# Performance work log

Measured on AMD Instinct MI355X. Metric: run time of the kernel, lower is better.

The kernel has to match this reference:

```python
import jax, jax.numpy as jnp
import numpy as np

NOISE_EPS = 1e-2


def setup_inputs() -> dict:
    key = jax.random.key(0)
    ks = jax.random.split(key, 6)
    N, D, E, H = 16384, 512, 8, 1024
    x = jax.random.normal(ks[0], (N, D), jnp.float32)
    eps = jax.random.normal(ks[1], (N, E), jnp.float32)
    w_gate = jax.random.normal(ks[2], (D, E), jnp.float32) * 0.02
    w_noise = jax.random.normal(ks[3], (D, E), jnp.float32) * 0.02
    W_h = jnp.eye(E, dtype=jnp.float32)  # module initializes W_h = eye(num_experts)
    W1 = jax.random.normal(ks[4], (E, D, H), jnp.float32) * 0.02
    b1 = jnp.zeros((E, H), jnp.float32)
    W2 = jax.random.normal(ks[5], (E, H, D), jnp.float32) * 0.02
    b2 = jnp.zeros((E, D), jnp.float32)
    return dict(x=x, eps=eps, w_gate=w_gate, w_noise=w_noise, W_h=W_h,
                W1=W1, b1=b1, W2=W2, b2=b2, k=2, capacity=5120)


def reference(x, eps, w_gate, w_noise, W_h, W1, b1, W2, b2, k, capacity):
    N, D = x.shape
    E = w_gate.shape[1]
    # --- noisy top-k gating ---
    clean_logits = (x @ w_gate) @ W_h                       # [N, E]
    noise_stddev = jax.nn.softplus(x @ w_noise) + NOISE_EPS  # [N, E]
    noisy_logits = clean_logits + eps * noise_stddev
    top_vals, top_idx = jax.lax.top_k(noisy_logits, k)       # [N, k]
    top_gates = jax.nn.softmax(top_vals, axis=-1)
    gates = jnp.zeros((N, E), x.dtype).at[jnp.arange(N)[:, None], top_idx].set(top_gates)
    # --- capacity masking: keep the first `capacity` routed tokens per expert (batch order) ---
    active = gates > 0
    rank = jnp.cumsum(active, axis=0) - 1                    # per-expert arrival rank
    keep = active & (rank < capacity)
    gates = jnp.where(keep, gates, jnp.zeros((), x.dtype))
    # --- dispatch into fixed [E, capacity] buffers (dummy slot absorbs dropped writes) ---
    flat = jnp.where(keep, jnp.arange(E)[None, :] * capacity + rank, E * capacity)  # [N, E]
    tok = jnp.broadcast_to(jnp.arange(N, dtype=jnp.int32)[:, None], (N, E))
    buf = jnp.zeros(E * capacity + 1, jnp.int32).at[flat].set(tok)[:E * capacity].reshape(E, capacity)
    gbuf = jnp.zeros(E * capacity + 1, x.dtype).at[flat].set(gates)[:E * capacity].reshape(E, capacity)
    x_exp = x[buf]                                           # [E, C, D] gather
    # --- per-expert 1-layer FFN (grouped GEMM) ---
    h = jax.nn.relu(jnp.einsum('ecd,edh->ech', x_exp, W1) + b1[:, None, :])
    y_exp = jnp.einsum('ech,eho->eco', h, W2) + b2[:, None, :]
    # --- weighted scatter-combine (unfilled slots have gate 0, so they add nothing) ---
    weighted = y_exp * gbuf[..., None]
    combined = jnp.zeros((N, D), x.dtype).at[buf.reshape(-1)].add(weighted.reshape(-1, D))
    return combined
```

## Files before the change

kernel.cpp:

```cpp
#include <hip/hip_runtime.h>
#include <hip/hip_bf16.h>
#include <cstdint>

#define NTOK 16384
#define DIM 512
#define NEXP 8
#define HID 1024
#define CAPACITY 5120

typedef __attribute__((ext_vector_type(8))) short bf16x8;
typedef __attribute__((ext_vector_type(4))) float f32x4;
typedef unsigned long long u64;

__device__ __forceinline__ unsigned short f2bf(float f) {
    unsigned u = __float_as_uint(f);
    unsigned r = (u + 0x7FFFu + ((u >> 16) & 1u)) >> 16;
    return (unsigned short)r;
}

#define GLDS16(gp, lp) __builtin_amdgcn_global_load_lds( \
    (const __attribute__((address_space(1))) void*)(gp), \
    (__attribute__((address_space(3))) void*)(lp), 16, 0, 0)

__global__ __launch_bounds__(256) void gating_kernel(
    const float* __restrict__ x, const float* __restrict__ eps,
    const float* __restrict__ wg, const float* __restrict__ wn,
    const float* __restrict__ Wh, int2* __restrict__ rec)
{
    int w = threadIdx.x >> 6, lane = threadIdx.x & 63;
    int n = blockIdx.x * 4 + w;
    float ag[8], an[8];
#pragma unroll
    for (int e = 0; e < 8; ++e) { ag[e] = 0.f; an[e] = 0.f; }
    const float* xr = x + (size_t)n * DIM;
#pragma unroll
    for (int i = 0; i < DIM / 64; ++i) {
        int d = i * 64 + lane;
        float xv = xr[d];
        const float4* g4 = reinterpret_cast<const float4*>(wg + (size_t)d * 8);
        const float4* n4 = reinterpret_cast<const float4*>(wn + (size_t)d * 8);
        float4 a0 = g4[0], a1 = g4[1], b0 = n4[0], b1v = n4[1];
        ag[0] += xv * a0.x; ag[1] += xv * a0.y; ag[2] += xv * a0.z; ag[3] += xv * a0.w;
        ag[4] += xv * a1.x; ag[5] += xv * a1.y; ag[6] += xv * a1.z; ag[7] += xv * a1.w;
        an[0] += xv * b0.x; an[1] += xv * b0.y; an[2] += xv * b0.z; an[3] += xv * b0.w;
        an[4] += xv * b1v.x; an[5] += xv * b1v.y; an[6] += xv * b1v.z; an[7] += xv * b1v.w;
    }
#pragma unroll
    for (int off = 32; off; off >>= 1) {
#pragma unroll
        for (int e = 0; e < 8; ++e) {
            ag[e] += __shfl_xor(ag[e], off);
            an[e] += __shfl_xor(an[e], off);
        }
    }
    float noisy[8];
#pragma unroll
    for (int e = 0; e < 8; ++e) {
        float c = 0.f;
#pragma unroll
        for (int j = 0; j < 8; ++j) c += ag[j] * Wh[j * 8 + e];
        float v = an[e];
        float sp = fmaxf(v, 0.f) + log1pf(expf(-fabsf(v)));
        noisy[e] = c + eps[(size_t)n * 8 + e] * (sp + 1e-2f);
    }
    int i1 = 0; float v1 = noisy[0];
#pragma unroll
    for (int e = 1; e < 8; ++e) if (noisy[e] > v1) { v1 = noisy[e]; i1 = e; }
    int i2 = -1; float v2 = -3.4e38f;
#pragma unroll
    for (int e = 0; e < 8; ++e) if (e != i1 && noisy[e] > v2) { v2 = noisy[e]; i2 = e; }
    float ex = expf(v2 - v1);
    float g1 = 1.f / (1.f + ex);
    if (lane == 0)
        rec[n] = make_int2(i1 | (i2 << 8), __float_as_int(g1));
}

__global__ __launch_bounds__(1024) void scan_local(
    const int2* __restrict__ rec, unsigned* __restrict__ lrank, int* __restrict__ btot)
{
    __shared__ u64 wtot[16];
    __shared__ int wprefix[16][8];
    int tid = threadIdx.x, w = tid >> 6, lane = tid & 63;
    int n = blockIdx.x * 1024 + tid;
    int2 r = rec[n];
    int e1 = r.x & 0xFF, e2 = (r.x >> 8) & 0xFF;
    u64 m = (1ULL << (e1 * 8)) | (1ULL << (e2 * 8));
    u64 incl = m;
#pragma unroll
    for (int off = 1; off < 64; off <<= 1) {
        u64 v = __shfl_up(incl, off);
        if (lane >= off) incl += v;
    }
    if (lane == 63) wtot[w] = incl;
    __syncthreads();
    if (tid < 128) {
        int e = tid & 7, ww = tid >> 3;
        int s = 0;
        for (int j = 0; j < ww; ++j) s += (int)((wtot[j] >> (e * 8)) & 0xFF);
        wprefix[ww][e] = s;
        if (ww == 15)
            btot[blockIdx.x * 8 + e] = s + (int)((wtot[15] >> (e * 8)) & 0xFF);
    }
    __syncthreads();
    u64 excl = incl - m;
    unsigned l1 = (unsigned)(wprefix[w][e1] + (int)((excl >> (e1 * 8)) & 0xFF));
    unsigned l2 = (unsigned)(wprefix[w][e2] + (int)((excl >> (e2 * 8)) & 0xFF));
    lrank[n] = l1 | (l2 << 16);
}

__global__ __launch_bounds__(64) void scan_offs(
    const int* __restrict__ btot, int* __restrict__ off, int* __restrict__ counts,
    const int* __restrict__ cap_p)
{
    int e = threadIdx.x;
    if (e >= 8) return;
    int cap = *cap_p; if (cap > CAPACITY) cap = CAPACITY;
    int run = 0;
    for (int b = 0; b < 16; ++b) {
        off[b * 8 + e] = run;
        run += btot[b * 8 + e];
    }
    counts[e] = min(run, cap);
}

__global__ __launch_bounds__(1024) void scatter_k(
    const int2* __restrict__ rec, const unsigned* __restrict__ lrank,
    const int* __restrict__ off, const int* __restrict__ cap_p,
    int* __restrict__ buf, float* __restrict__ gbuf)
{
    int tid = threadIdx.x, b = blockIdx.x;
    int n = b * 1024 + tid;
    int cap = *cap_p; if (cap > CAPACITY) cap = CAPACITY;
    int2 r = rec[n];
    int e1 = r.x & 0xFF, e2 = (r.x >> 8) & 0xFF;
    float g1 = __int_as_float(r.y), g2 = 1.f - g1;
    unsigned lr = lrank[n];
    int r1 = off[b * 8 + e1] + (int)(lr & 0xFFFF);
    int r2 = off[b * 8 + e2] + (int)(lr >> 16);
    if (r1 < cap) { buf[e1 * CAPACITY + r1] = n; gbuf[e1 * CAPACITY + r1] = g1; }
    if (r2 < cap) { buf[e2 * CAPACITY + r2] = n; gbuf[e2 * CAPACITY + r2] = g2; }
}

__global__ __launch_bounds__(256) void gather_x(
    const float* __restrict__ x, const int* __restrict__ buf,
    const int* __restrict__ counts, unsigned short* __restrict__ xe)
{
    int slot = blockIdx.x * 4 + (threadIdx.x >> 6);
    int d0 = (threadIdx.x & 63) * 8;
    int e = slot / CAPACITY, rr = slot - e * CAPACITY;
    int4 v = make_int4(0, 0, 0, 0);
    if (rr < counts[e]) {
        int tok = buf[slot];
        const float* src = x + (size_t)tok * DIM + d0;
        float4 a = *reinterpret_cast<const float4*>(src);
        float4 b = *reinterpret_cast<const float4*>(src + 4);
        v.x = f2bf(a.x) | ((int)f2bf(a.y) << 16);
        v.y = f2bf(a.z) | ((int)f2bf(a.w) << 16);
        v.z = f2bf(b.x) | ((int)f2bf(b.y) << 16);
        v.w = f2bf(b.z) | ((int)f2bf(b.w) << 16);
    }
    *reinterpret_cast<int4*>(xe + (size_t)slot * DIM + d0) = v;
}

__global__ __launch_bounds__(256) void tcvt(const float* __restrict__ in,
                                            unsigned short* __restrict__ out, int R, int C)
{
    __shared__ float tile[32][33];
    int z = blockIdx.z;
    int c0 = blockIdx.x * 32, r0 = blockIdx.y * 32;
    int tx = threadIdx.x, ty = threadIdx.y;
    const float* inz = in + (size_t)z * R * C;
    unsigned short* outz = out + (size_t)z * R * C;
#pragma unroll
    for (int j = 0; j < 32; j += 8)
        tile[ty + j][tx] = inz[(size_t)(r0 + ty + j) * C + c0 + tx];
    __syncthreads();
#pragma unroll
    for (int j = 0; j < 32; j += 8)
        outz[(size_t)(c0 + ty + j) * R + r0 + tx] = f2bf(tile[tx][ty + j]);
}

template <int MODE>
__global__ __launch_bounds__(256, 4) void ffn_gemm(
    const unsigned short* __restrict__ A, const unsigned short* __restrict__ Bt,
    const float* __restrict__ bias, unsigned short* __restrict__ Hout,
    float* __restrict__ Out, const int* __restrict__ buf,
    const float* __restrict__ gbuf, const int* __restrict__ counts,
    int Ka, int Nd)
{
    int flat = blockIdx.x + gridDim.x * (blockIdx.y + gridDim.y * blockIdx.z);
    int e  = flat & 7;
    int rr = flat >> 3;
    int tn = rr % gridDim.y;
    int tm = rr / gridDim.y;

    int cnt = counts[e];
    if (tm * 128 >= cnt) return;
    int tid = threadIdx.x, w = tid >> 6, lane = tid & 63;
    int q = lane >> 4, rl = lane & 15;

    __shared__ __align__(16) char lds[32768];
    char* As = lds;
    char* Bs = lds + 16384;

    unsigned aoff[4], boff[4];
#pragma unroll
    for (int i = 0; i < 4; ++i) {
        int p = (w * 4 + i) * 64 + lane;
        int row = p >> 3, kp = p & 7;
        int c = kp ^ (row & 7);
        aoff[i] = (unsigned)(e * CAPACITY + tm * 128 + row) * Ka + c * 8;
        boff[i] = (unsigned)(e * Nd + tn * 128 + row) * Ka + c * 8;
    }

    f32x4 acc[4][4];
#pragma unroll
    for (int mi = 0; mi < 4; ++mi)
#pragma unroll
        for (int ni = 0; ni < 4; ++ni)
            acc[mi][ni] = (f32x4){0.f, 0.f, 0.f, 0.f};

    int wm = w >> 1, wn = w & 1;

    for (int k0 = 0; k0 < Ka; k0 += 64) {
#pragma unroll
        for (int i = 0; i < 4; ++i) {
            GLDS16(A + aoff[i] + k0, As + (w * 4 + i) * 1024);
            GLDS16(Bt + boff[i] + k0, Bs + (w * 4 + i) * 1024);
        }
        __syncthreads();
#pragma unroll
        for (int kk = 0; kk < 2; ++kk) {
            bf16x8 af[4], bfr[4];
#pragma unroll
            for (int mi = 0; mi < 4; ++mi) {
                int row = wm * 64 + mi * 16 + rl;
                int cc = (kk * 4 + q) ^ (row & 7);
                af[mi] = *reinterpret_cast<const bf16x8*>(As + row * 128 + cc * 16);
            }
#pragma unroll
            for (int ni = 0; ni < 4; ++ni) {
                int row = wn * 64 + ni * 16 + rl;
                int cc = (kk * 4 + q) ^ (row & 7);
                bfr[ni] = *reinterpret_cast<const bf16x8*>(Bs + row * 128 + cc * 16);
            }
#pragma unroll
            for (int mi = 0; mi < 4; ++mi)
#pragma unroll
                for (int ni = 0; ni < 4; ++ni)
                    acc[mi][ni] = __builtin_amdgcn_mfma_f32_16x16x32_bf16(
                        af[mi], bfr[ni], acc[mi][ni], 0, 0, 0);
        }
        __syncthreads();
    }

    if (MODE == 1) {
#pragma unroll
        for (int ni = 0; ni < 4; ++ni) {
            int gcol = tn * 128 + wn * 64 + ni * 16 + rl;
            float bv = bias[e * Nd + gcol];
#pragma unroll
            for (int mi = 0; mi < 4; ++mi) {
#pragma unroll
                for (int r = 0; r < 4; ++r) {
                    int grow = tm * 128 + wm * 64 + mi * 16 + q * 4 + r;
                    float v = fmaxf(acc[mi][ni][r] + bv, 0.f);
                    Hout[(size_t)(e * CAPACITY + grow) * HID + gcol] = f2bf(v);
                }
            }
        }
    } else {
        int ebase = e * CAPACITY;
#pragma unroll
        for (int ni = 0; ni < 4; ++ni) {
            int gcol = tn * 128 + wn * 64 + ni * 16 + rl;
            float bv = bias[e * Nd + gcol];
#pragma unroll
            for (int mi = 0; mi < 4; ++mi) {
#pragma unroll
                for (int r = 0; r < 4; ++r) {
                    int grow = tm * 128 + wm * 64 + mi * 16 + q * 4 + r;
                    if (grow < cnt) {
                        int tok = buf[ebase + grow];
                        float g = gbuf[ebase + grow];
                        float v = (acc[mi][ni][r] + bv) * g;
                        atomicAdd(Out + (size_t)tok * DIM + gcol, v);
                    }
                }
            }
        }
    }
}

extern "C" void kernel_launch(void* const* d_in, const int* in_sizes, int n_in,
                              void* d_out, int out_size, void* d_ws, size_t ws_size,
                              hipStream_t stream)
{
    const float* x   = (const float*)d_in[0];
    const float* eps = (const float*)d_in[1];
    const float* wg  = (const float*)d_in[2];
    const float* wn  = (const float*)d_in[3];
    const float* Wh  = (const float*)d_in[4];
    const float* W1  = (const float*)d_in[5];
    const float* b1  = (const float*)d_in[6];
    const float* W2  = (const float*)d_in[7];
    const float* b2  = (const float*)d_in[8];
    const int* capp  = (const int*)d_in[10];

    char* ws = (char*)d_ws;
    unsigned short* xe   = (unsigned short*)(ws);
    unsigned short* w1t  = (unsigned short*)(ws + 41943040);
    unsigned short* w2t  = (unsigned short*)(ws + 50331648);
    unsigned short* hK   = (unsigned short*)(ws + 58720256);
    int*      buf    = (int*)     (ws + 142606336);
    float*    gbuf   = (float*)   (ws + 142770176);
    int2*     rec    = (int2*)    (ws + 142934016);
    unsigned* lrank  = (unsigned*)(ws + 143065088);
    int*      btot   = (int*)     (ws + 143130624);
    int*      off    = (int*)     (ws + 143131136);
    int*      counts = (int*)     (ws + 143131648);

    float* out = (float*)d_out;
    hipMemsetAsync(out, 0, (size_t)out_size * sizeof(float), stream);

    gating_kernel<<<NTOK / 4, 256, 0, stream>>>(x, eps, wg, wn, Wh, rec);
    scan_local<<<16, 1024, 0, stream>>>(rec, lrank, btot);
    scan_offs<<<1, 64, 0, stream>>>(btot, off, counts, capp);
    scatter_k<<<16, 1024, 0, stream>>>(rec, lrank, off, capp, buf, gbuf);
    tcvt<<<dim3(HID / 32, DIM / 32, NEXP), dim3(32, 8), 0, stream>>>(W1, w1t, DIM, HID);
    tcvt<<<dim3(DIM / 32, HID / 32, NEXP), dim3(32, 8), 0, stream>>>(W2, w2t, HID, DIM);
    gather_x<<<NEXP * CAPACITY / 4, 256, 0, stream>>>(x, buf, counts, xe);

    ffn_gemm<1><<<dim3(CAPACITY / 128, HID / 128, NEXP), 256, 0, stream>>>(
        xe, w1t, b1, hK, nullptr, buf, gbuf, counts, DIM, HID);
    ffn_gemm<0><<<dim3(CAPACITY / 128, DIM / 128, NEXP), 256, 0, stream>>>(
        hK, w2t, b2, nullptr, out, buf, gbuf, counts, HID, DIM);
}
```

Measured before the change: 245.9 us.

## Use 256x128 GEMM tiles with 8 waves and a K-step of 32

The expert FFN GEMM now uses 512-thread blocks (8 waves) that each cover 256 rows by 128 columns, and the K step drops from 64 to 32. LDS shrinks to 24 KB and the XOR swizzle is redone for the 64-byte rows. The larger M tile means each B tile loaded from global memory is reused by more rows. In exchange there are twice as many barriers per unit of K, less work per synchronization, and fewer blocks in the grid. A partially filled expert also does more wasted compute, because the early exit now only skips whole 256-row tiles.

```diff
diff --git a/kernel.cpp b/kernel.cpp
--- a/kernel.cpp
+++ b/kernel.cpp
@@ -181,7 +181,7 @@
 }
 
 template <int MODE>
-__global__ __launch_bounds__(256, 4) void ffn_gemm(
+__global__ __launch_bounds__(512, 4) void ffn_gemm(
     const unsigned short* __restrict__ A, const unsigned short* __restrict__ Bt,
     const float* __restrict__ bias, unsigned short* __restrict__ Hout,
     float* __restrict__ Out, const int* __restrict__ buf,
@@ -195,22 +195,28 @@
     int tm = rr / gridDim.y;
 
     int cnt = counts[e];
-    if (tm * 128 >= cnt) return;
+    if (tm * 256 >= cnt) return;
     int tid = threadIdx.x, w = tid >> 6, lane = tid & 63;
     int q = lane >> 4, rl = lane & 15;
-
-    __shared__ __align__(16) char lds[32768];
-    char* As = lds;
-    char* Bs = lds + 16384;
-
-    unsigned aoff[4], boff[4];
-#pragma unroll
-    for (int i = 0; i < 4; ++i) {
-        int p = (w * 4 + i) * 64 + lane;
-        int row = p >> 3, kp = p & 7;
-        int c = kp ^ (row & 7);
-        aoff[i] = (unsigned)(e * CAPACITY + tm * 128 + row) * Ka + c * 8;
-        boff[i] = (unsigned)(e * Nd + tn * 128 + row) * Ka + c * 8;
+    int wm = w >> 1, wn = w & 1;
+
+    __shared__ __align__(16) char lds[24576];
+    char* Alds = lds;
+    char* Blds = lds + 16384;
+
+    unsigned aoff0, aoff1, boff0;
+    {
+        int p0 = tid;
+        int r0 = p0 >> 2, kp0 = p0 & 3;
+        int kc0 = kp0 ^ ((r0 >> 1) & 3);
+        aoff0 = (unsigned)(e * CAPACITY + tm * 256 + r0) * Ka + kc0 * 8;
+        int p1 = tid + 512;
+        int r1 = p1 >> 2, kp1 = p1 & 3;
+        int kc1 = kp1 ^ ((r1 >> 1) & 3);
+        aoff1 = (unsigned)(e * CAPACITY + tm * 256 + r1) * Ka + kc1 * 8;
+        int rb = tid >> 2, kpb = tid & 3;
+        int kcb = kpb ^ ((rb >> 1) & 3);
+        boff0 = (unsigned)(e * Nd + tn * 128 + rb) * Ka + kcb * 8;
     }
 
     f32x4 acc[4][4];
@@ -220,37 +226,32 @@
         for (int ni = 0; ni < 4; ++ni)
             acc[mi][ni] = (f32x4){0.f, 0.f, 0.f, 0.f};
 
-    int wm = w >> 1, wn = w & 1;
-
-    for (int k0 = 0; k0 < Ka; k0 += 64) {
-#pragma unroll
-        for (int i = 0; i < 4; ++i) {
-            GLDS16(A + aoff[i] + k0, As + (w * 4 + i) * 1024);
-            GLDS16(Bt + boff[i] + k0, Bs + (w * 4 + i) * 1024);
-        }
+    int cc = (q ^ ((rl >> 1) & 3)) << 4;
+    int nkt = Ka >> 5;
+
+    for (int t = 0; t < nkt; ++t) {
+        int k0 = t * 32;
+        GLDS16(A + aoff0 + k0, Alds + tid * 16);
+        GLDS16(A + aoff1 + k0, Alds + tid * 16 + 8192);
+        GLDS16(Bt + boff0 + k0, Blds + tid * 16);
         __syncthreads();
-#pragma unroll
-        for (int kk = 0; kk < 2; ++kk) {
-            bf16x8 af[4], bfr[4];
-#pragma unroll
-            for (int mi = 0; mi < 4; ++mi) {
-                int row = wm * 64 + mi * 16 + rl;
-                int cc = (kk * 4 + q) ^ (row & 7);
-                af[mi] = *reinterpret_cast<const bf16x8*>(As + row * 128 + cc * 16);
-            }
-#pragma unroll
-            for (int ni = 0; ni < 4; ++ni) {
-                int row = wn * 64 + ni * 16 + rl;
-                int cc = (kk * 4 + q) ^ (row & 7);
-                bfr[ni] = *reinterpret_cast<const bf16x8*>(Bs + row * 128 + cc * 16);
-            }
-#pragma unroll
-            for (int mi = 0; mi < 4; ++mi)
-#pragma unroll
-                for (int ni = 0; ni < 4; ++ni)
-                    acc[mi][ni] = __builtin_amdgcn_mfma_f32_16x16x32_bf16(
-                        af[mi], bfr[ni], acc[mi][ni], 0, 0, 0);
-        }
+        bf16x8 af[4], bfr[4];
+#pragma unroll
+        for (int mi = 0; mi < 4; ++mi) {
+            int row = wm * 64 + mi * 16 + rl;
+            af[mi] = *reinterpret_cast<const bf16x8*>(Alds + row * 64 + cc);
+        }
+#pragma unroll
+        for (int ni = 0; ni < 4; ++ni) {
+            int row = wn * 64 + ni * 16 + rl;
+            bfr[ni] = *reinterpret_cast<const bf16x8*>(Blds + row * 64 + cc);
+        }
+#pragma unroll
+        for (int mi = 0; mi < 4; ++mi)
+#pragma unroll
+            for (int ni = 0; ni < 4; ++ni)
+                acc[mi][ni] = __builtin_amdgcn_mfma_f32_16x16x32_bf16(
+                    af[mi], bfr[ni], acc[mi][ni], 0, 0, 0);
         __syncthreads();
     }
 
@@ -263,7 +264,7 @@
             for (int mi = 0; mi < 4; ++mi) {
 #pragma unroll
                 for (int r = 0; r < 4; ++r) {
-                    int grow = tm * 128 + wm * 64 + mi * 16 + q * 4 + r;
+                    int grow = tm * 256 + wm * 64 + mi * 16 + q * 4 + r;
                     float v = fmaxf(acc[mi][ni][r] + bv, 0.f);
                     Hout[(size_t)(e * CAPACITY + grow) * HID + gcol] = f2bf(v);
                 }
@@ -279,7 +280,7 @@
             for (int mi = 0; mi < 4; ++mi) {
 #pragma unroll
                 for (int r = 0; r < 4; ++r) {
-                    int grow = tm * 128 + wm * 64 + mi * 16 + q * 4 + r;
+                    int grow = tm * 256 + wm * 64 + mi * 16 + q * 4 + r;
                     if (grow < cnt) {
                         int tok = buf[ebase + grow];
                         float g = gbuf[ebase + grow];
@@ -331,8 +332,8 @@
     tcvt<<<dim3(DIM / 32, HID / 32, NEXP), dim3(32, 8), 0, stream>>>(W2, w2t, HID, DIM);
     gather_x<<<NEXP * CAPACITY / 4, 256, 0, stream>>>(x, buf, counts, xe);
 
-    ffn_gemm<1><<<dim3(CAPACITY / 128, HID / 128, NEXP), 256, 0, stream>>>(
+    ffn_gemm<1><<<dim3(CAPACITY / 256, HID / 128, NEXP), 512, 0, stream>>>(
         xe, w1t, b1, hK, nullptr, buf, gbuf, counts, DIM, HID);
-    ffn_gemm<0><<<dim3(CAPACITY / 128, DIM / 128, NEXP), 256, 0, stream>>>(
+    ffn_gemm<0><<<dim3(CAPACITY / 256, DIM / 128, NEXP), 512, 0, stream>>>(
         hK, w2t, b2, nullptr, out, buf, gbuf, counts, HID, DIM);
 }
```

Measured after the change: 273.2 us. +11.1%, slower.

## Fuse token gather into first GEMM loads and split-K the second GEMM

Applied to the files above, without the earlier changes.

The separate gather_x kernel is replaced by a dense conversion of x to bf16, and the first FFN GEMM reads token rows indirectly through buf when it computes its global-to-LDS addresses. This removes the materialised [E, capacity, D] gathered buffer and its extra write and read. The second GEMM now splits K into two halves with twice as many blocks, and the bias is added only by the first half, since results are already combined with atomics. The cost is that all 16384 tokens are converted rather than only routed slots, atomic traffic on the output doubles, and A-tile loads for the first GEMM become scattered rows.

```diff
diff --git a/kernel.cpp b/kernel.cpp
--- a/kernel.cpp
+++ b/kernel.cpp
@@ -141,25 +141,19 @@
     if (r2 < cap) { buf[e2 * CAPACITY + r2] = n; gbuf[e2 * CAPACITY + r2] = g2; }
 }
 
-__global__ __launch_bounds__(256) void gather_x(
-    const float* __restrict__ x, const int* __restrict__ buf,
-    const int* __restrict__ counts, unsigned short* __restrict__ xe)
-{
-    int slot = blockIdx.x * 4 + (threadIdx.x >> 6);
-    int d0 = (threadIdx.x & 63) * 8;
-    int e = slot / CAPACITY, rr = slot - e * CAPACITY;
-    int4 v = make_int4(0, 0, 0, 0);
-    if (rr < counts[e]) {
-        int tok = buf[slot];
-        const float* src = x + (size_t)tok * DIM + d0;
-        float4 a = *reinterpret_cast<const float4*>(src);
-        float4 b = *reinterpret_cast<const float4*>(src + 4);
-        v.x = f2bf(a.x) | ((int)f2bf(a.y) << 16);
-        v.y = f2bf(a.z) | ((int)f2bf(a.w) << 16);
-        v.z = f2bf(b.x) | ((int)f2bf(b.y) << 16);
-        v.w = f2bf(b.z) | ((int)f2bf(b.w) << 16);
-    }
-    *reinterpret_cast<int4*>(xe + (size_t)slot * DIM + d0) = v;
+__global__ __launch_bounds__(256) void cvt_x(const float* __restrict__ in,
+                                             unsigned short* __restrict__ out, int n)
+{
+    int i = (blockIdx.x * 256 + threadIdx.x) * 8;
+    if (i >= n) return;
+    float4 a = *reinterpret_cast<const float4*>(in + i);
+    float4 b = *reinterpret_cast<const float4*>(in + i + 4);
+    int4 v;
+    v.x = f2bf(a.x) | ((int)f2bf(a.y) << 16);
+    v.y = f2bf(a.z) | ((int)f2bf(a.w) << 16);
+    v.z = f2bf(b.x) | ((int)f2bf(b.y) << 16);
+    v.w = f2bf(b.z) | ((int)f2bf(b.w) << 16);
+    *reinterpret_cast<int4*>(out + i) = v;
 }
 
 __global__ __launch_bounds__(256) void tcvt(const float* __restrict__ in,
@@ -191,13 +185,17 @@
     int flat = blockIdx.x + gridDim.x * (blockIdx.y + gridDim.y * blockIdx.z);
     int e  = flat & 7;
     int rr = flat >> 3;
-    int tn = rr % gridDim.y;
-    int tm = rr / gridDim.y;
+    int q8 = rr % 8;
+    int tm = rr / 8;
+    int tn, kh;
+    if (MODE == 0) { tn = q8 >> 1; kh = q8 & 1; }
+    else           { tn = q8;      kh = 0; }
 
     int cnt = counts[e];
     if (tm * 128 >= cnt) return;
     int tid = threadIdx.x, w = tid >> 6, lane = tid & 63;
     int q = lane >> 4, rl = lane & 15;
+    int ebase = e * CAPACITY;
 
     __shared__ __align__(16) char lds[32768];
     char* As = lds;
@@ -209,7 +207,13 @@
         int p = (w * 4 + i) * 64 + lane;
         int row = p >> 3, kp = p & 7;
         int c = kp ^ (row & 7);
-        aoff[i] = (unsigned)(e * CAPACITY + tm * 128 + row) * Ka + c * 8;
+        int slot = tm * 128 + row;
+        if (MODE == 1) {
+            int tok = (slot < cnt) ? buf[ebase + slot] : 0;
+            aoff[i] = (unsigned)tok * Ka + c * 8;
+        } else {
+            aoff[i] = (unsigned)(ebase + slot) * Ka + c * 8;
+        }
         boff[i] = (unsigned)(e * Nd + tn * 128 + row) * Ka + c * 8;
     }
 
@@ -221,8 +225,10 @@
             acc[mi][ni] = (f32x4){0.f, 0.f, 0.f, 0.f};
 
     int wm = w >> 1, wn = w & 1;
-
-    for (int k0 = 0; k0 < Ka; k0 += 64) {
+    int kbeg = (MODE == 0) ? kh * (Ka >> 1) : 0;
+    int kend = kbeg + ((MODE == 0) ? (Ka >> 1) : Ka);
+
+    for (int k0 = kbeg; k0 < kend; k0 += 64) {
 #pragma unroll
         for (int i = 0; i < 4; ++i) {
             GLDS16(A + aoff[i] + k0, As + (w * 4 + i) * 1024);
@@ -265,16 +271,15 @@
                 for (int r = 0; r < 4; ++r) {
                     int grow = tm * 128 + wm * 64 + mi * 16 + q * 4 + r;
                     float v = fmaxf(acc[mi][ni][r] + bv, 0.f);
-                    Hout[(size_t)(e * CAPACITY + grow) * HID + gcol] = f2bf(v);
+                    Hout[(size_t)(ebase + grow) * HID + gcol] = f2bf(v);
                 }
             }
         }
     } else {
-        int ebase = e * CAPACITY;
 #pragma unroll
         for (int ni = 0; ni < 4; ++ni) {
             int gcol = tn * 128 + wn * 64 + ni * 16 + rl;
-            float bv = bias[e * Nd + gcol];
+            float bv = kh ? 0.f : bias[e * Nd + gcol];
 #pragma unroll
             for (int mi = 0; mi < 4; ++mi) {
 #pragma unroll
@@ -308,7 +313,7 @@
     const int* capp  = (const int*)d_in[10];
 
     char* ws = (char*)d_ws;
-    unsigned short* xe   = (unsigned short*)(ws);
+    unsigned short* xg   = (unsigned short*)(ws);
     unsigned short* w1t  = (unsigned short*)(ws + 41943040);
     unsigned short* w2t  = (unsigned short*)(ws + 50331648);
     unsigned short* hK   = (unsigned short*)(ws + 58720256);
@@ -327,12 +332,12 @@
     scan_local<<<16, 1024, 0, stream>>>(rec, lrank, btot);
     scan_offs<<<1, 64, 0, stream>>>(btot, off, counts, capp);
     scatter_k<<<16, 1024, 0, stream>>>(rec, lrank, off, capp, buf, gbuf);
+    cvt_x<<<NTOK * DIM / 8 / 256, 256, 0, stream>>>(x, xg, NTOK * DIM);
     tcvt<<<dim3(HID / 32, DIM / 32, NEXP), dim3(32, 8), 0, stream>>>(W1, w1t, DIM, HID);
     tcvt<<<dim3(DIM / 32, HID / 32, NEXP), dim3(32, 8), 0, stream>>>(W2, w2t, HID, DIM);
-    gather_x<<<NEXP * CAPACITY / 4, 256, 0, stream>>>(x, buf, counts, xe);
 
     ffn_gemm<1><<<dim3(CAPACITY / 128, HID / 128, NEXP), 256, 0, stream>>>(
-        xe, w1t, b1, hK, nullptr, buf, gbuf, counts, DIM, HID);
-    ffn_gemm<0><<<dim3(CAPACITY / 128, DIM / 128, NEXP), 256, 0, stream>>>(
+        xg, w1t, b1, hK, nullptr, buf, gbuf, counts, DIM, HID);
+    ffn_gemm<0><<<dim3(CAPACITY / 128, 8, NEXP), 256, 0, stream>>>(
         hK, w2t, b2, nullptr, out, buf, gbuf, counts, HID, DIM);
 }
```

Measured after the change: 276.5 us. +12.5%, slower.
